# Kernel optimization log

Measured on AMD Instinct MI355X. Metric: run time of the kernel, lower is better.

The kernel has to match this reference:

```python
import jax, jax.numpy as jnp
import numpy as np

DT = 0.001
TAU_INV = 1.0 / 0.006   # tau_mem_inv == tau_syn_inv for both cells
V_TH = 1.0              # norse defaults: v_leak=0, v_reset=0


def heaviside(x):
    return (x > 0).astype(x.dtype)


def setup_inputs() -> dict:
    key = jax.random.key(0)
    k1, k2, k3 = jax.random.split(key, 3)
    T, B, I, H, O = 128, 2048, 64, 256, 16
    inp = jax.random.normal(k1, (T, B, I), dtype=jnp.float32)
    # torch.nn.Linear default init ~ U(-1/sqrt(fan_in), 1/sqrt(fan_in))
    w1 = jax.random.uniform(k2, (H, I), jnp.float32, -1.0, 1.0) / np.sqrt(I)
    w2 = jax.random.uniform(k3, (O, H), jnp.float32, -1.0, 1.0) / np.sqrt(H)
    return {"input": inp, "w1": w1, "w2": w2}


def _snn_forward(inp, w1, w2):
    B = inp.shape[1]
    H, O = w1.shape[0], w2.shape[0]
    decay = 1.0 - DT * TAU_INV

    def step(carry, x_t):
        v1, i1, v2, i2 = carry
        # LIF cell (hidden layer)
        g1 = x_t @ w1.T                              # [B, H]
        v_dec = v1 + DT * TAU_INV * (i1 - v1)        # Euler membrane update
        i_dec = i1 * decay                           # synaptic decay
        z = heaviside(v_dec - V_TH)                  # spikes
        v1n = (1.0 - z) * v_dec                      # reset to 0 where spiked
        i1n = i_dec + g1
        # LI cell (readout)
        g2 = z @ w2.T                                # [B, O]
        v2n = v2 + DT * TAU_INV * (i2 - v2)
        i2n = i2 * decay + g2
        return (v1n, i1n, v2n, i2n), (z, v2n)

    init = (jnp.zeros((B, H), inp.dtype), jnp.zeros((B, H), inp.dtype),
            jnp.zeros((B, O), inp.dtype), jnp.zeros((B, O), inp.dtype))
    _, (zs, ys) = jax.lax.scan(step, init, inp)
    score = jnp.max(ys, axis=0)                      # amax over time -> [B, O]
    spikes_mean = jnp.mean(jnp.sum(zs, axis=(0, 2)))
    return score, spikes_mean


def reference(input, w1, w2):
    return _snn_forward(input, w1, w2)
```

## Files before the change

kernel.cpp:

```cpp
#include <hip/hip_runtime.h>
#include <hip/hip_bf16.h>

#define T_STEPS 128
#define BATCH   2048
#define IN_F    64
#define HID     256
#define OUT_F   16
#define CH      16
#define TROWS   16
#define HHALF   128
#define NCHUNK  (T_STEPS / CH)
#define SLAB    (BATCH * OUT_F)

typedef __attribute__((ext_vector_type(8))) short bf16x8;
typedef __attribute__((ext_vector_type(4))) float f32x4;
typedef unsigned short u16;
typedef unsigned int   u32;

__device__ __forceinline__ u16 f2bf(float f) {
    union { __hip_bfloat16 h; u16 u; } cv;
    cv.h = __float2bfloat16(f);
    return cv.u;
}
__device__ __forceinline__ float bf2f(u16 h) {
    return __uint_as_float(((u32)h) << 16);
}
__device__ __forceinline__ bf16x8 pack8(float4 a, float4 b) {
    bf16x8 r;
    r[0] = (short)f2bf(a.x); r[1] = (short)f2bf(a.y);
    r[2] = (short)f2bf(a.z); r[3] = (short)f2bf(a.w);
    r[4] = (short)f2bf(b.x); r[5] = (short)f2bf(b.y);
    r[6] = (short)f2bf(b.z); r[7] = (short)f2bf(b.w);
    return r;
}

__global__ void snn_init_kernel(float* __restrict__ out) {
    if (threadIdx.x == 0 && blockIdx.x == 0) out[BATCH * OUT_F] = 0.0f;
}

__global__ void __launch_bounds__(512, 2)
snn_l1_kernel(const float* __restrict__ x, const float* __restrict__ w1,
              const float* __restrict__ w2, u16* __restrict__ g2p,
              float* __restrict__ out)
{
    const int tid  = threadIdx.x;
    const int lane = tid & 63;
    const int wv   = tid >> 6;
    const int hi   = lane >> 4;
    const int l15  = lane & 15;
    const int tile = blockIdx.x & 127;
    const int half = blockIdx.x >> 7;
    const int row0 = tile * TROWS;

    __shared__ __attribute__((aligned(16))) u16 xl[CH * TROWS * IN_F];
    __shared__ __attribute__((aligned(16))) u16 zb[CH * TROWS * HHALF];
    __shared__ float sacc;
    if (tid == 0) sacc = 0.f;

    const f32x4 zf = {0.f, 0.f, 0.f, 0.f};
    const float dt_tau = (float)(0.001 * (1.0 / 0.006));
    const float decay  = (float)(1.0 - 0.001 * (1.0 / 0.006));

    const int hcol = half * HHALF + wv * 16 + l15;
    bf16x8 w1f[2];
#pragma unroll
    for (int kt = 0; kt < 2; ++kt)
        w1f[kt] = pack8(*(const float4*)&w1[hcol * IN_F + kt * 32 + hi * 8],
                        *(const float4*)&w1[hcol * IN_F + kt * 32 + hi * 8 + 4]);

    bf16x8 w2f[4];
#pragma unroll
    for (int kt = 0; kt < 4; ++kt) {
        const int k0 = half * HHALF + kt * 32 + hi * 8;
        w2f[kt] = pack8(*(const float4*)&w2[l15 * HID + k0],
                        *(const float4*)&w2[l15 * HID + k0 + 4]);
    }

    int wofs[4];
    const float* gp[4];
    const size_t cstride = (size_t)CH * BATCH * IN_F;
#pragma unroll
    for (int j = 0; j < 4; ++j) {
        const int v  = tid + 512 * j;
        const int vs = v >> 7;
        const int vr = (v >> 3) & 15;
        const int vk = (v & 7) * 8;
        wofs[j] = (vs * TROWS + vr) * IN_F + (vk ^ ((vr & 7) << 3));
        gp[j]   = x + ((size_t)vs * BATCH + row0 + vr) * IN_F + vk;
    }
    float4 ra[4], rb[4];
#pragma unroll
    for (int j = 0; j < 4; ++j) {
        ra[j] = *(const float4*)gp[j];
        rb[j] = *(const float4*)(gp[j] + 4);
        *(bf16x8*)&xl[wofs[j]] = pack8(ra[j], rb[j]);
    }
#pragma unroll
    for (int j = 0; j < 4; ++j) {
        ra[j] = *(const float4*)(gp[j] + cstride);
        rb[j] = *(const float4*)(gp[j] + cstride + 4);
    }

    f32x4 v1 = zf, i1 = zf;
    int wcnt = 0;
    const int xswz = (l15 & 7) << 3;
    int zoff[4];
#pragma unroll
    for (int r = 0; r < 4; ++r) {
        const int zr = 4 * hi + r;
        zoff[r] = zr * HHALF + ((wv * 16 + l15) ^ ((zr & 15) << 3));
    }
    __syncthreads();

    for (int c = 0; c < NCHUNK; ++c) {
        f32x4 g1[CH];
#pragma unroll
        for (int s = 0; s < CH; ++s) {
            const u16* xrow = &xl[(s * TROWS + l15) * IN_F];
            const bf16x8 xf0 = *(const bf16x8*)(xrow + ((hi * 8) ^ xswz));
            const bf16x8 xf1 = *(const bf16x8*)(xrow + ((32 + hi * 8) ^ xswz));
            g1[s] = __builtin_amdgcn_mfma_f32_16x16x32_bf16(xf0, w1f[0], zf, 0, 0, 0);
            g1[s] = __builtin_amdgcn_mfma_f32_16x16x32_bf16(xf1, w1f[1], g1[s], 0, 0, 0);
        }

#pragma unroll
        for (int s = 0; s < CH; ++s) {
            u16* zw = &zb[s * TROWS * HHALF];
            const f32x4 vd = v1 + dt_tau * (i1 - v1);
            const f32x4 id = i1 * decay;
#pragma unroll
            for (int r = 0; r < 4; ++r) {
                const bool sp = vd[r] > 1.0f;
                v1[r] = sp ? 0.f : vd[r];
                wcnt += __popcll(__ballot(sp));
                zw[zoff[r]] = sp ? (u16)0x3F80 : (u16)0;
            }
            i1 = id + g1[s];
        }

        __syncthreads();

        if (c + 1 < NCHUNK) {
#pragma unroll
            for (int j = 0; j < 4; ++j)
                *(bf16x8*)&xl[wofs[j]] = pack8(ra[j], rb[j]);
            if (c + 2 < NCHUNK) {
#pragma unroll
                for (int j = 0; j < 4; ++j) {
                    const float* g = gp[j] + 2 * cstride;
                    ra[j] = *(const float4*)g;
                    rb[j] = *(const float4*)(g + 4);
                    gp[j] += cstride;
                }
            }
        }

#pragma unroll
        for (int ss = 0; ss < 2; ++ss) {
            const int s = ss * 8 + wv;
            const u16* zr2 = &zb[(s * TROWS + l15) * HHALF];
            const int rsw = l15 << 3;
            const bf16x8 z0 = *(const bf16x8*)(zr2 + ((0 * 32 + hi * 8) ^ rsw));
            const bf16x8 z1 = *(const bf16x8*)(zr2 + ((1 * 32 + hi * 8) ^ rsw));
            const bf16x8 z2 = *(const bf16x8*)(zr2 + ((2 * 32 + hi * 8) ^ rsw));
            const bf16x8 z3 = *(const bf16x8*)(zr2 + ((3 * 32 + hi * 8) ^ rsw));
            f32x4 ga = __builtin_amdgcn_mfma_f32_16x16x32_bf16(z0, w2f[0], zf, 0, 0, 0);
            f32x4 gb = __builtin_amdgcn_mfma_f32_16x16x32_bf16(z1, w2f[1], zf, 0, 0, 0);
            ga = __builtin_amdgcn_mfma_f32_16x16x32_bf16(z2, w2f[2], ga, 0, 0, 0);
            gb = __builtin_amdgcn_mfma_f32_16x16x32_bf16(z3, w2f[3], gb, 0, 0, 0);
            const f32x4 g2 = ga + gb;
            u16* dst = g2p + (size_t)half * (T_STEPS * SLAB)
                     + (size_t)(c * CH + s) * SLAB + (row0 + 4 * hi) * OUT_F + l15;
#pragma unroll
            for (int r = 0; r < 4; ++r) dst[r * OUT_F] = f2bf(g2[r]);
        }

        __syncthreads();
    }

    if (lane == 0) atomicAdd(&sacc, (float)wcnt);
    __syncthreads();
    if (tid == 0) atomicAdd(&out[BATCH * OUT_F], sacc * (1.0f / BATCH));
}

__global__ void __launch_bounds__(128)
snn_li_kernel(const u16* __restrict__ g2p, float* __restrict__ out)
{
    const int gid = blockIdx.x * 128 + threadIdx.x;
    const u16* p0 = g2p + gid;
    const u16* p1 = g2p + (size_t)T_STEPS * SLAB + gid;
    const float dt_tau = (float)(0.001 * (1.0 / 0.006));
    const float decay  = (float)(1.0 - 0.001 * (1.0 / 0.006));
    float v2 = 0.f, i2 = 0.f, ymax = -1e30f;
#pragma unroll 8
    for (int t = 0; t < T_STEPS; ++t) {
        const float g = bf2f(p0[(size_t)t * SLAB]) + bf2f(p1[(size_t)t * SLAB]);
        v2 = fmaf(dt_tau, i2 - v2, v2);
        ymax = fmaxf(ymax, v2);
        i2 = i2 * decay + g;
    }
    out[gid] = ymax;
}

extern "C" void kernel_launch(void* const* d_in, const int* in_sizes, int n_in,
                              void* d_out, int out_size, void* d_ws, size_t ws_size,
                              hipStream_t stream) {
    const float* x  = (const float*)d_in[0];
    const float* w1 = (const float*)d_in[1];
    const float* w2 = (const float*)d_in[2];
    float* out = (float*)d_out;
    u16* g2p = (u16*)d_ws;

    hipLaunchKernelGGL(snn_init_kernel, dim3(1), dim3(64), 0, stream, out);
    hipLaunchKernelGGL(snn_l1_kernel, dim3(256), dim3(512), 0, stream,
                       x, w1, w2, g2p, out);
    hipLaunchKernelGGL(snn_li_kernel, dim3(BATCH * OUT_F / 128), dim3(128), 0,
                       stream, g2p, out);
}
```

Baseline: 55.45 us.

## Split hidden layer into quarters with double-buffered LDS and one barrier per chunk

```diff
diff --git a/kernel.cpp b/kernel.cpp
--- a/kernel.cpp
+++ b/kernel.cpp
@@ -6,9 +6,10 @@
 #define IN_F    64
 #define HID     256
 #define OUT_F   16
-#define CH      16
+#define CH      8
 #define TROWS   16
-#define HHALF   128
+#define HQ      64
+#define NQ      4
 #define NCHUNK  (T_STEPS / CH)
 #define SLAB    (BATCH * OUT_F)
 
@@ -38,7 +39,7 @@
     if (threadIdx.x == 0 && blockIdx.x == 0) out[BATCH * OUT_F] = 0.0f;
 }
 
-__global__ void __launch_bounds__(512, 2)
+__global__ void __launch_bounds__(256, 2)
 snn_l1_kernel(const float* __restrict__ x, const float* __restrict__ w1,
               const float* __restrict__ w2, u16* __restrict__ g2p,
               float* __restrict__ out)
@@ -49,11 +50,12 @@
     const int hi   = lane >> 4;
     const int l15  = lane & 15;
     const int tile = blockIdx.x & 127;
-    const int half = blockIdx.x >> 7;
+    const int quarter = blockIdx.x >> 7;
     const int row0 = tile * TROWS;
-
-    __shared__ __attribute__((aligned(16))) u16 xl[CH * TROWS * IN_F];
-    __shared__ __attribute__((aligned(16))) u16 zb[CH * TROWS * HHALF];
+    const int hbase = quarter * HQ;
+
+    __shared__ __attribute__((aligned(16))) u16 xl[2][CH * TROWS * IN_F];
+    __shared__ __attribute__((aligned(16))) u16 zb[2][CH * TROWS * HQ];
     __shared__ float sacc;
     if (tid == 0) sacc = 0.f;
 
@@ -61,17 +63,17 @@
     const float dt_tau = (float)(0.001 * (1.0 / 0.006));
     const float decay  = (float)(1.0 - 0.001 * (1.0 / 0.006));
 
-    const int hcol = half * HHALF + wv * 16 + l15;
+    const int hcol = hbase + wv * 16 + l15;
     bf16x8 w1f[2];
 #pragma unroll
     for (int kt = 0; kt < 2; ++kt)
         w1f[kt] = pack8(*(const float4*)&w1[hcol * IN_F + kt * 32 + hi * 8],
                         *(const float4*)&w1[hcol * IN_F + kt * 32 + hi * 8 + 4]);
 
-    bf16x8 w2f[4];
-#pragma unroll
-    for (int kt = 0; kt < 4; ++kt) {
-        const int k0 = half * HHALF + kt * 32 + hi * 8;
+    bf16x8 w2f[2];
+#pragma unroll
+    for (int kt = 0; kt < 2; ++kt) {
+        const int k0 = hbase + kt * 32 + hi * 8;
         w2f[kt] = pack8(*(const float4*)&w2[l15 * HID + k0],
                         *(const float4*)&w2[l15 * HID + k0 + 4]);
     }
@@ -81,7 +83,7 @@
     const size_t cstride = (size_t)CH * BATCH * IN_F;
 #pragma unroll
     for (int j = 0; j < 4; ++j) {
-        const int v  = tid + 512 * j;
+        const int v  = tid + 256 * j;
         const int vs = v >> 7;
         const int vr = (v >> 3) & 15;
         const int vk = (v & 7) * 8;
@@ -93,12 +95,13 @@
     for (int j = 0; j < 4; ++j) {
         ra[j] = *(const float4*)gp[j];
         rb[j] = *(const float4*)(gp[j] + 4);
-        *(bf16x8*)&xl[wofs[j]] = pack8(ra[j], rb[j]);
+        *(bf16x8*)&xl[0][wofs[j]] = pack8(ra[j], rb[j]);
     }
 #pragma unroll
     for (int j = 0; j < 4; ++j) {
         ra[j] = *(const float4*)(gp[j] + cstride);
         rb[j] = *(const float4*)(gp[j] + cstride + 4);
+        gp[j] += 2 * cstride;
     }
 
     f32x4 v1 = zf, i1 = zf;
@@ -108,24 +111,31 @@
 #pragma unroll
     for (int r = 0; r < 4; ++r) {
         const int zr = 4 * hi + r;
-        zoff[r] = zr * HHALF + ((wv * 16 + l15) ^ ((zr & 15) << 3));
+        zoff[r] = zr * HQ + ((wv * 16 + l15) ^ ((zr & 7) << 3));
     }
     __syncthreads();
 
     for (int c = 0; c < NCHUNK; ++c) {
+        const int p = c & 1;
+
         f32x4 g1[CH];
 #pragma unroll
         for (int s = 0; s < CH; ++s) {
-            const u16* xrow = &xl[(s * TROWS + l15) * IN_F];
+            const u16* xrow = &xl[p][(s * TROWS + l15) * IN_F];
             const bf16x8 xf0 = *(const bf16x8*)(xrow + ((hi * 8) ^ xswz));
             const bf16x8 xf1 = *(const bf16x8*)(xrow + ((32 + hi * 8) ^ xswz));
             g1[s] = __builtin_amdgcn_mfma_f32_16x16x32_bf16(xf0, w1f[0], zf, 0, 0, 0);
             g1[s] = __builtin_amdgcn_mfma_f32_16x16x32_bf16(xf1, w1f[1], g1[s], 0, 0, 0);
         }
 
+        if (c + 1 < NCHUNK) {
+#pragma unroll
+            for (int j = 0; j < 4; ++j)
+                *(bf16x8*)&xl[p ^ 1][wofs[j]] = pack8(ra[j], rb[j]);
+        }
 #pragma unroll
         for (int s = 0; s < CH; ++s) {
-            u16* zw = &zb[s * TROWS * HHALF];
+            u16* zw = &zb[p][s * TROWS * HQ];
             const f32x4 vd = v1 + dt_tau * (i1 - v1);
             const f32x4 id = i1 * decay;
 #pragma unroll
@@ -140,42 +150,27 @@
 
         __syncthreads();
 
-        if (c + 1 < NCHUNK) {
-#pragma unroll
-            for (int j = 0; j < 4; ++j)
-                *(bf16x8*)&xl[wofs[j]] = pack8(ra[j], rb[j]);
-            if (c + 2 < NCHUNK) {
-#pragma unroll
-                for (int j = 0; j < 4; ++j) {
-                    const float* g = gp[j] + 2 * cstride;
-                    ra[j] = *(const float4*)g;
-                    rb[j] = *(const float4*)(g + 4);
-                    gp[j] += cstride;
-                }
+        if (c + 2 < NCHUNK) {
+#pragma unroll
+            for (int j = 0; j < 4; ++j) {
+                ra[j] = *(const float4*)gp[j];
+                rb[j] = *(const float4*)(gp[j] + 4);
+                gp[j] += cstride;
             }
         }
-
 #pragma unroll
         for (int ss = 0; ss < 2; ++ss) {
-            const int s = ss * 8 + wv;
-            const u16* zr2 = &zb[(s * TROWS + l15) * HHALF];
-            const int rsw = l15 << 3;
-            const bf16x8 z0 = *(const bf16x8*)(zr2 + ((0 * 32 + hi * 8) ^ rsw));
-            const bf16x8 z1 = *(const bf16x8*)(zr2 + ((1 * 32 + hi * 8) ^ rsw));
-            const bf16x8 z2 = *(const bf16x8*)(zr2 + ((2 * 32 + hi * 8) ^ rsw));
-            const bf16x8 z3 = *(const bf16x8*)(zr2 + ((3 * 32 + hi * 8) ^ rsw));
-            f32x4 ga = __builtin_amdgcn_mfma_f32_16x16x32_bf16(z0, w2f[0], zf, 0, 0, 0);
-            f32x4 gb = __builtin_amdgcn_mfma_f32_16x16x32_bf16(z1, w2f[1], zf, 0, 0, 0);
-            ga = __builtin_amdgcn_mfma_f32_16x16x32_bf16(z2, w2f[2], ga, 0, 0, 0);
-            gb = __builtin_amdgcn_mfma_f32_16x16x32_bf16(z3, w2f[3], gb, 0, 0, 0);
-            const f32x4 g2 = ga + gb;
-            u16* dst = g2p + (size_t)half * (T_STEPS * SLAB)
+            const int s = ss * 4 + wv;
+            const u16* zr2 = &zb[p][(s * TROWS + l15) * HQ];
+            const bf16x8 z0 = *(const bf16x8*)(zr2 + ((hi * 8) ^ xswz));
+            const bf16x8 z1 = *(const bf16x8*)(zr2 + ((32 + hi * 8) ^ xswz));
+            f32x4 g2 = __builtin_amdgcn_mfma_f32_16x16x32_bf16(z0, w2f[0], zf, 0, 0, 0);
+            g2 = __builtin_amdgcn_mfma_f32_16x16x32_bf16(z1, w2f[1], g2, 0, 0, 0);
+            u16* dst = g2p + (size_t)quarter * (T_STEPS * SLAB)
                      + (size_t)(c * CH + s) * SLAB + (row0 + 4 * hi) * OUT_F + l15;
 #pragma unroll
             for (int r = 0; r < 4; ++r) dst[r * OUT_F] = f2bf(g2[r]);
         }
-
-        __syncthreads();
     }
 
     if (lane == 0) atomicAdd(&sacc, (float)wcnt);
@@ -183,18 +178,21 @@
     if (tid == 0) atomicAdd(&out[BATCH * OUT_F], sacc * (1.0f / BATCH));
 }
 
-__global__ void __launch_bounds__(128)
+__global__ void __launch_bounds__(256)
 snn_li_kernel(const u16* __restrict__ g2p, float* __restrict__ out)
 {
-    const int gid = blockIdx.x * 128 + threadIdx.x;
+    const int gid = blockIdx.x * 256 + threadIdx.x;
     const u16* p0 = g2p + gid;
-    const u16* p1 = g2p + (size_t)T_STEPS * SLAB + gid;
+    const u16* p1 = p0 + (size_t)T_STEPS * SLAB;
+    const u16* p2 = p1 + (size_t)T_STEPS * SLAB;
+    const u16* p3 = p2 + (size_t)T_STEPS * SLAB;
     const float dt_tau = (float)(0.001 * (1.0 / 0.006));
     const float decay  = (float)(1.0 - 0.001 * (1.0 / 0.006));
     float v2 = 0.f, i2 = 0.f, ymax = -1e30f;
 #pragma unroll 8
     for (int t = 0; t < T_STEPS; ++t) {
-        const float g = bf2f(p0[(size_t)t * SLAB]) + bf2f(p1[(size_t)t * SLAB]);
+        const size_t o = (size_t)t * SLAB;
+        const float g = (bf2f(p0[o]) + bf2f(p1[o])) + (bf2f(p2[o]) + bf2f(p3[o]));
         v2 = fmaf(dt_tau, i2 - v2, v2);
         ymax = fmaxf(ymax, v2);
         i2 = i2 * decay + g;
@@ -212,8 +210,8 @@
     u16* g2p = (u16*)d_ws;
 
     hipLaunchKernelGGL(snn_init_kernel, dim3(1), dim3(64), 0, stream, out);
-    hipLaunchKernelGGL(snn_l1_kernel, dim3(256), dim3(512), 0, stream,
+    hipLaunchKernelGGL(snn_l1_kernel, dim3(128 * NQ), dim3(256), 0, stream,
                        x, w1, w2, g2p, out);
-    hipLaunchKernelGGL(snn_li_kernel, dim3(BATCH * OUT_F / 128), dim3(128), 0,
+    hipLaunchKernelGGL(snn_li_kernel, dim3(BATCH * OUT_F / 256), dim3(256), 0,
                        stream, g2p, out);
 }
```

New measurement: 56.75 us. 1.02x slower.

## Load input straight into MFMA fragments and compute layer-2 partials per wave in registers

Applied to the files above, without the earlier changes.

```diff
diff --git a/kernel.cpp b/kernel.cpp
--- a/kernel.cpp
+++ b/kernel.cpp
@@ -6,11 +6,12 @@
 #define IN_F    64
 #define HID     256
 #define OUT_F   16
-#define CH      16
+#define CH      8
 #define TROWS   16
 #define HHALF   128
-#define NCHUNK  (T_STEPS / CH)
+#define NCH     (T_STEPS / CH)
 #define SLAB    (BATCH * OUT_F)
+#define PD      4
 
 typedef __attribute__((ext_vector_type(8))) short bf16x8;
 typedef __attribute__((ext_vector_type(4))) float f32x4;
@@ -38,7 +39,7 @@
     if (threadIdx.x == 0 && blockIdx.x == 0) out[BATCH * OUT_F] = 0.0f;
 }
 
-__global__ void __launch_bounds__(512, 2)
+__global__ void __launch_bounds__(256, 1)
 snn_l1_kernel(const float* __restrict__ x, const float* __restrict__ w1,
               const float* __restrict__ w2, u16* __restrict__ g2p,
               float* __restrict__ out)
@@ -51,9 +52,9 @@
     const int tile = blockIdx.x & 127;
     const int half = blockIdx.x >> 7;
     const int row0 = tile * TROWS;
-
-    __shared__ __attribute__((aligned(16))) u16 xl[CH * TROWS * IN_F];
-    __shared__ __attribute__((aligned(16))) u16 zb[CH * TROWS * HHALF];
+    const int hbase = half * HHALF + wv * 32;
+
+    __shared__ __attribute__((aligned(16))) float ws[2][CH][4][256];
     __shared__ float sacc;
     if (tid == 0) sacc = 0.f;
 
@@ -61,121 +62,101 @@
     const float dt_tau = (float)(0.001 * (1.0 / 0.006));
     const float decay  = (float)(1.0 - 0.001 * (1.0 / 0.006));
 
-    const int hcol = half * HHALF + wv * 16 + l15;
-    bf16x8 w1f[2];
-#pragma unroll
-    for (int kt = 0; kt < 2; ++kt)
-        w1f[kt] = pack8(*(const float4*)&w1[hcol * IN_F + kt * 32 + hi * 8],
-                        *(const float4*)&w1[hcol * IN_F + kt * 32 + hi * 8 + 4]);
-
-    bf16x8 w2f[4];
-#pragma unroll
-    for (int kt = 0; kt < 4; ++kt) {
-        const int k0 = half * HHALF + kt * 32 + hi * 8;
-        w2f[kt] = pack8(*(const float4*)&w2[l15 * HID + k0],
-                        *(const float4*)&w2[l15 * HID + k0 + 4]);
-    }
-
-    int wofs[4];
-    const float* gp[4];
-    const size_t cstride = (size_t)CH * BATCH * IN_F;
-#pragma unroll
-    for (int j = 0; j < 4; ++j) {
-        const int v  = tid + 512 * j;
-        const int vs = v >> 7;
-        const int vr = (v >> 3) & 15;
-        const int vk = (v & 7) * 8;
-        wofs[j] = (vs * TROWS + vr) * IN_F + (vk ^ ((vr & 7) << 3));
-        gp[j]   = x + ((size_t)vs * BATCH + row0 + vr) * IN_F + vk;
-    }
-    float4 ra[4], rb[4];
-#pragma unroll
-    for (int j = 0; j < 4; ++j) {
-        ra[j] = *(const float4*)gp[j];
-        rb[j] = *(const float4*)(gp[j] + 4);
-        *(bf16x8*)&xl[wofs[j]] = pack8(ra[j], rb[j]);
-    }
-#pragma unroll
-    for (int j = 0; j < 4; ++j) {
-        ra[j] = *(const float4*)(gp[j] + cstride);
-        rb[j] = *(const float4*)(gp[j] + cstride + 4);
-    }
-
-    f32x4 v1 = zf, i1 = zf;
+    bf16x8 w1f[2][2];
+#pragma unroll
+    for (int tt = 0; tt < 2; ++tt)
+#pragma unroll
+        for (int kh = 0; kh < 2; ++kh) {
+            const float* src = &w1[(hbase + tt * 16 + l15) * IN_F + kh * 32 + hi * 8];
+            w1f[tt][kh] = pack8(*(const float4*)src, *(const float4*)(src + 4));
+        }
+
+    bf16x8 w2f;
+#pragma unroll
+    for (int i = 0; i < 8; ++i) {
+        const int h = hbase + ((i < 4) ? (4 * hi + i) : (16 + 4 * hi + (i - 4)));
+        w2f[i] = (short)f2bf(w2[l15 * HID + h]);
+    }
+
+    const size_t tstride = (size_t)BATCH * IN_F;
+    const float* xp[PD];
+    float4 ra[PD], rb[PD], rc[PD], rd[PD];
+#pragma unroll
+    for (int j = 0; j < PD; ++j) {
+        xp[j] = x + (size_t)j * tstride + (row0 + l15) * IN_F + hi * 8;
+        ra[j] = *(const float4*)(xp[j]);
+        rb[j] = *(const float4*)(xp[j] + 4);
+        rc[j] = *(const float4*)(xp[j] + 32);
+        rd[j] = *(const float4*)(xp[j] + 36);
+    }
+
+    f32x4 v1[2] = {zf, zf}, i1[2] = {zf, zf};
     int wcnt = 0;
-    const int xswz = (l15 & 7) << 3;
-    int zoff[4];
-#pragma unroll
-    for (int r = 0; r < 4; ++r) {
-        const int zr = 4 * hi + r;
-        zoff[r] = zr * HHALF + ((wv * 16 + l15) ^ ((zr & 15) << 3));
-    }
+    int pb = 0;
     __syncthreads();
 
-    for (int c = 0; c < NCHUNK; ++c) {
-        f32x4 g1[CH];
+    for (int c = 0; c < NCH; ++c) {
 #pragma unroll
         for (int s = 0; s < CH; ++s) {
-            const u16* xrow = &xl[(s * TROWS + l15) * IN_F];
-            const bf16x8 xf0 = *(const bf16x8*)(xrow + ((hi * 8) ^ xswz));
-            const bf16x8 xf1 = *(const bf16x8*)(xrow + ((32 + hi * 8) ^ xswz));
-            g1[s] = __builtin_amdgcn_mfma_f32_16x16x32_bf16(xf0, w1f[0], zf, 0, 0, 0);
-            g1[s] = __builtin_amdgcn_mfma_f32_16x16x32_bf16(xf1, w1f[1], g1[s], 0, 0, 0);
+            const int j = s & (PD - 1);
+            const int t = c * CH + s;
+
+            const bf16x8 xf0 = pack8(ra[j], rb[j]);
+            const bf16x8 xf1 = pack8(rc[j], rd[j]);
+            f32x4 g1[2];
+#pragma unroll
+            for (int tt = 0; tt < 2; ++tt) {
+                g1[tt] = __builtin_amdgcn_mfma_f32_16x16x32_bf16(w1f[tt][0], xf0, zf, 0, 0, 0);
+                g1[tt] = __builtin_amdgcn_mfma_f32_16x16x32_bf16(w1f[tt][1], xf1, g1[tt], 0, 0, 0);
+            }
+
+            if (t + PD < T_STEPS) {
+                xp[j] += PD * tstride;
+                ra[j] = *(const float4*)(xp[j]);
+                rb[j] = *(const float4*)(xp[j] + 4);
+                rc[j] = *(const float4*)(xp[j] + 32);
+                rd[j] = *(const float4*)(xp[j] + 36);
+            }
+
+            u32 zi[4];
+#pragma unroll
+            for (int tt = 0; tt < 2; ++tt) {
+                const f32x4 vd = v1[tt] + dt_tau * (i1[tt] - v1[tt]);
+                bool sp[4];
+#pragma unroll
+                for (int r = 0; r < 4; ++r) {
+                    sp[r] = vd[r] > 1.0f;
+                    v1[tt][r] = sp[r] ? 0.f : vd[r];
+                    wcnt += __popcll(__ballot(sp[r]));
+                }
+                zi[2 * tt]     = (sp[0] ? 0x3F80u : 0u) | (sp[1] ? 0x3F800000u : 0u);
+                zi[2 * tt + 1] = (sp[2] ? 0x3F80u : 0u) | (sp[3] ? 0x3F800000u : 0u);
+                i1[tt] = i1[tt] * decay + g1[tt];
+            }
+            union { u32 u[4]; bf16x8 v; } zz;
+            zz.u[0] = zi[0]; zz.u[1] = zi[1]; zz.u[2] = zi[2]; zz.u[3] = zi[3];
+
+            const f32x4 p = __builtin_amdgcn_mfma_f32_16x16x32_bf16(zz.v, w2f, zf, 0, 0, 0);
+            *(f32x4*)&ws[pb][s][wv][lane * 4] = p;
         }
 
-#pragma unroll
-        for (int s = 0; s < CH; ++s) {
-            u16* zw = &zb[s * TROWS * HHALF];
-            const f32x4 vd = v1 + dt_tau * (i1 - v1);
-            const f32x4 id = i1 * decay;
-#pragma unroll
-            for (int r = 0; r < 4; ++r) {
-                const bool sp = vd[r] > 1.0f;
-                v1[r] = sp ? 0.f : vd[r];
-                wcnt += __popcll(__ballot(sp));
-                zw[zoff[r]] = sp ? (u16)0x3F80 : (u16)0;
-            }
-            i1 = id + g1[s];
-        }
-
         __syncthreads();
 
-        if (c + 1 < NCHUNK) {
-#pragma unroll
-            for (int j = 0; j < 4; ++j)
-                *(bf16x8*)&xl[wofs[j]] = pack8(ra[j], rb[j]);
-            if (c + 2 < NCHUNK) {
-#pragma unroll
-                for (int j = 0; j < 4; ++j) {
-                    const float* g = gp[j] + 2 * cstride;
-                    ra[j] = *(const float4*)g;
-                    rb[j] = *(const float4*)(g + 4);
-                    gp[j] += cstride;
-                }
-            }
-        }
-
-#pragma unroll
-        for (int ss = 0; ss < 2; ++ss) {
-            const int s = ss * 8 + wv;
-            const u16* zr2 = &zb[(s * TROWS + l15) * HHALF];
-            const int rsw = l15 << 3;
-            const bf16x8 z0 = *(const bf16x8*)(zr2 + ((0 * 32 + hi * 8) ^ rsw));
-            const bf16x8 z1 = *(const bf16x8*)(zr2 + ((1 * 32 + hi * 8) ^ rsw));
-            const bf16x8 z2 = *(const bf16x8*)(zr2 + ((2 * 32 + hi * 8) ^ rsw));
-            const bf16x8 z3 = *(const bf16x8*)(zr2 + ((3 * 32 + hi * 8) ^ rsw));
-            f32x4 ga = __builtin_amdgcn_mfma_f32_16x16x32_bf16(z0, w2f[0], zf, 0, 0, 0);
-            f32x4 gb = __builtin_amdgcn_mfma_f32_16x16x32_bf16(z1, w2f[1], zf, 0, 0, 0);
-            ga = __builtin_amdgcn_mfma_f32_16x16x32_bf16(z2, w2f[2], ga, 0, 0, 0);
-            gb = __builtin_amdgcn_mfma_f32_16x16x32_bf16(z3, w2f[3], gb, 0, 0, 0);
-            const f32x4 g2 = ga + gb;
+#pragma unroll
+        for (int q = 0; q < 2; ++q) {
+            const int s = wv * 2 + q;
+            const float* wp = &ws[pb][s][0][lane * 4];
+            const f32x4 a0 = *(const f32x4*)(wp);
+            const f32x4 a1 = *(const f32x4*)(wp + 256);
+            const f32x4 a2 = *(const f32x4*)(wp + 512);
+            const f32x4 a3 = *(const f32x4*)(wp + 768);
+            const f32x4 g2 = (a0 + a1) + (a2 + a3);
             u16* dst = g2p + (size_t)half * (T_STEPS * SLAB)
                      + (size_t)(c * CH + s) * SLAB + (row0 + 4 * hi) * OUT_F + l15;
 #pragma unroll
             for (int r = 0; r < 4; ++r) dst[r * OUT_F] = f2bf(g2[r]);
         }
-
-        __syncthreads();
+        pb ^= 1;
     }
 
     if (lane == 0) atomicAdd(&sacc, (float)wcnt);
@@ -188,13 +169,14 @@
 {
     const int gid = blockIdx.x * 128 + threadIdx.x;
     const u16* p0 = g2p + gid;
-    const u16* p1 = g2p + (size_t)T_STEPS * SLAB + gid;
+    const u16* p1 = p0 + (size_t)T_STEPS * SLAB;
     const float dt_tau = (float)(0.001 * (1.0 / 0.006));
     const float decay  = (float)(1.0 - 0.001 * (1.0 / 0.006));
     float v2 = 0.f, i2 = 0.f, ymax = -1e30f;
 #pragma unroll 8
     for (int t = 0; t < T_STEPS; ++t) {
-        const float g = bf2f(p0[(size_t)t * SLAB]) + bf2f(p1[(size_t)t * SLAB]);
+        const size_t o = (size_t)t * SLAB;
+        const float g = bf2f(p0[o]) + bf2f(p1[o]);
         v2 = fmaf(dt_tau, i2 - v2, v2);
         ymax = fmaxf(ymax, v2);
         i2 = i2 * decay + g;
@@ -212,7 +194,7 @@
     u16* g2p = (u16*)d_ws;
 
     hipLaunchKernelGGL(snn_init_kernel, dim3(1), dim3(64), 0, stream, out);
-    hipLaunchKernelGGL(snn_l1_kernel, dim3(256), dim3(512), 0, stream,
+    hipLaunchKernelGGL(snn_l1_kernel, dim3(256), dim3(256), 0, stream,
                        x, w1, w2, g2p, out);
     hipLaunchKernelGGL(snn_li_kernel, dim3(BATCH * OUT_F / 128), dim3(128), 0,
                        stream, g2p, out);
```

New measurement: 94.60 us. +70.6%, slower.
